# Kernel tuning notes

Hardware: AMD Instinct MI355X
Metric: run time of the kernel (lower is better)

## Reference

```python
import jax, jax.numpy as jnp
import numpy as np

N = 100000
E = 3_200_000
H = 64
R = 2
NEG = 0.01   # leaky_relu default slope
EPS = 1e-5   # BatchNorm eps


def leaky(x):
    return jnp.where(x > 0, x, NEG * x)


def bn(x, g, b, m, v):
    # BatchNorm1d in eval mode (running statistics)
    return (x - m) * jax.lax.rsqrt(v + EPS) * g + b


def setup_inputs() -> dict:
    key = jax.random.key(0)
    ks = jax.random.split(key, 16)
    d = {}
    d["des"] = jax.random.normal(ks[0], (N, 768), jnp.float32)
    d["num"] = jax.random.normal(ks[1], (N, 5), jnp.float32)
    d["cat"] = jax.random.normal(ks[2], (N, 6), jnp.float32)
    d["edge_index"] = jax.random.randint(ks[3], (2, E), 0, N)
    d["edge_type"] = jax.random.randint(ks[4], (E,), 0, R)

    def lin(k, o, i):
        return (jax.random.normal(k, (o, i), jnp.float32) / np.float32(np.sqrt(i)))

    # projection heads: Linear + BatchNorm1d params
    d["des_W"] = lin(ks[5], H, 768); d["des_b"] = jnp.zeros((H,), jnp.float32)
    d["num_W"] = lin(ks[6], H, 5);   d["num_b"] = jnp.zeros((H,), jnp.float32)
    d["cat_W"] = lin(ks[7], H, 6);   d["cat_b"] = jnp.zeros((H,), jnp.float32)
    for name, kk in (("des", ks[8]), ("num", ks[9]), ("cat", ks[10])):
        d[name + "_g"] = jnp.ones((H,), jnp.float32)
        d[name + "_beta"] = jnp.zeros((H,), jnp.float32)
        d[name + "_m"] = 0.1 * jax.random.normal(kk, (H,), jnp.float32)
        d[name + "_v"] = jnp.ones((H,), jnp.float32)
    # RGCN relation weights [R, in, out] (used as F.linear(x, W[r]) -> x @ W[r].T)
    d["rgcn_W"] = jax.random.normal(ks[11], (R, H, H), jnp.float32) / np.float32(np.sqrt(H))
    # classifier
    d["cls_W1"] = lin(ks[12], H // 2, H); d["cls_b1"] = jnp.zeros((H // 2,), jnp.float32)
    d["cls_W2"] = lin(ks[13], 2, H // 2); d["cls_b2"] = jnp.zeros((2,), jnp.float32)
    return d


def reference(des, num, cat, edge_index, edge_type,
              des_W, des_b, des_g, des_beta, des_m, des_v,
              num_W, num_b, num_g, num_beta, num_m, num_v,
              cat_W, cat_b, cat_g, cat_beta, cat_m, cat_v,
              rgcn_W, cls_W1, cls_b1, cls_W2, cls_b2):
    # feature fusion: three Linear+BN+LeakyReLU branches summed
    x = leaky(bn(des @ des_W.T + des_b, des_g, des_beta, des_m, des_v))
    x = x + leaky(bn(num @ num_W.T + num_b, num_g, num_beta, num_m, num_v))
    x = x + leaky(bn(cat @ cat_W.T + cat_b, cat_g, cat_beta, cat_m, cat_v))

    # SimpleRGCNConv: per-relation linear transform + masked scatter-mean over edges
    src, dst = edge_index[0], edge_index[1]  # PyG: row=source, col=target
    n = x.shape[0]
    acc = jnp.zeros((n, H), x.dtype)
    for r in range(R):
        x_r = x @ rgcn_W[r].T                       # F.linear(x, weight[r])
        mask = (edge_type == r).astype(x.dtype)     # [E]
        msg = x_r[src] * mask[:, None]              # gather + mask
        s = jax.ops.segment_sum(msg, dst, num_segments=n)
        cnt = jax.ops.segment_sum(mask, dst, num_segments=n)
        acc = acc + s / jnp.maximum(cnt, 1.0)[:, None]  # mean; 0 for isolated nodes
    x = leaky(acc / R)  # mean over relations

    # dropout in eval mode is identity; classifier
    h = leaky(x @ cls_W1.T + cls_b1)
    return h @ cls_W2.T + cls_b2
```

## Files before the change

### kernel.cpp

```cpp
#include <hip/hip_runtime.h>

typedef unsigned int u32;
typedef unsigned short u16;

#define NEG 0.01f
#define BN_EPS 1e-5f

typedef __attribute__((ext_vector_type(8))) short bf16x8;
typedef __attribute__((ext_vector_type(4))) float f32x4;

__device__ __forceinline__ float bl(u32 u){ union { u32 i; float f; } c; c.i = u << 16; return c.f; }
__device__ __forceinline__ float bh(u32 u){ union { u32 i; float f; } c; c.i = u & 0xFFFF0000u; return c.f; }
__device__ __forceinline__ u16 f2b(float f){
  union { float f; u32 i; } c; c.f = f;
  u32 t = c.i + 0x7FFFu + ((c.i >> 16) & 1u);
  return (u16)(t >> 16);
}
__device__ __forceinline__ float leaky(float v){ return v > 0.f ? v : NEG * v; }

__global__ __launch_bounds__(256) void k_hist_prep(
    const int* __restrict__ ei, const int* __restrict__ et, int E, int HB,
    int* __restrict__ deg2,
    const float* __restrict__ desWf, const float* __restrict__ rgcnW,
    const float* __restrict__ W1, u16* __restrict__ tab)
{
  int bid = blockIdx.x;
  if (bid < HB) {
    int e = bid * 256 + threadIdx.x;
    if (e < E) atomicAdd(&deg2[ei[E + e] * 2 + et[e]], 1);
  } else {
    int i = (bid - HB) * 256 + threadIdx.x;
    if (i < 49152) {
      int j = i & 7, lane = (i >> 3) & 63, t = (i >> 9) & 3, k = i >> 11;
      int row = 16 * t + (lane & 15);
      int col = 32 * k + 8 * (lane >> 4) + j;
      tab[i] = f2b(desWf[row * 768 + col]);
    } else if (i < 57344) {
      int j = i - 49152;
      int h = j >> 7, k = j & 127;
      tab[i] = f2b(rgcnW[(k >= 64 ? 4096 : 0) + h * 64 + (k & 63)]);
    } else if (i < 59392) {
      tab[i] = f2b(W1[i - 57344]);
    }
  }
}

__global__ __launch_bounds__(256) void k_scanA(
    const int* __restrict__ deg2, int* __restrict__ psum, int M)
{
  __shared__ int ws4[4];
  const int tid = threadIdx.x, lane = tid & 63, w = tid >> 6;
  int idx = blockIdx.x * 1024 + tid * 4;
  int4 v = {0, 0, 0, 0};
  if (idx < M) v = *(const int4*)(deg2 + idx);
  int s = v.x + v.y + v.z + v.w;
  #pragma unroll
  for (int o = 1; o < 64; o <<= 1) s += __shfl_xor(s, o);
  if (lane == 0) ws4[w] = s;
  __syncthreads();
  if (tid == 0) psum[blockIdx.x] = ws4[0] + ws4[1] + ws4[2] + ws4[3];
}

__global__ __launch_bounds__(256) void k_scanB(
    const int* __restrict__ psum, int* __restrict__ poff, int NCH)
{
  __shared__ int wsum[4];
  const int tid = threadIdx.x, lane = tid & 63, w = tid >> 6;
  int v = (tid < NCH) ? psum[tid] : 0;
  int s = v;
  #pragma unroll
  for (int o = 1; o < 64; o <<= 1) { int t = __shfl_up(s, o); if (lane >= o) s += t; }
  if (lane == 63) wsum[w] = s;
  __syncthreads();
  if (tid == 0) {
    int a = wsum[0];
    a += wsum[1]; wsum[1] = a;
    a += wsum[2]; wsum[2] = a;
    a += wsum[3]; wsum[3] = a;
  }
  __syncthreads();
  int wbase = (w == 0) ? 0 : wsum[w - 1];
  if (tid < NCH) poff[tid] = wbase + (s - v);
}

__global__ __launch_bounds__(256) void k_scanC(
    const int* __restrict__ deg2, const int* __restrict__ poff,
    int* __restrict__ offs2, int M, int E)
{
  __shared__ int wsum[4];
  const int tid = threadIdx.x, lane = tid & 63, w = tid >> 6;
  int idx = blockIdx.x * 1024 + tid * 4;
  int4 v = {0, 0, 0, 0};
  if (idx < M) v = *(const int4*)(deg2 + idx);
  int s4 = v.x + v.y + v.z + v.w;
  int s = s4;
  #pragma unroll
  for (int o = 1; o < 64; o <<= 1) { int t = __shfl_up(s, o); if (lane >= o) s += t; }
  if (lane == 63) wsum[w] = s;
  __syncthreads();
  if (tid == 0) {
    int a = wsum[0];
    a += wsum[1]; wsum[1] = a;
    a += wsum[2]; wsum[2] = a;
    a += wsum[3]; wsum[3] = a;
  }
  __syncthreads();
  int wbase = (w == 0) ? 0 : wsum[w - 1];
  int ebase = poff[blockIdx.x] + wbase + (s - s4);
  if (idx < M) {
    int4 o4;
    o4.x = ebase;
    o4.y = ebase + v.x;
    o4.z = ebase + v.x + v.y;
    o4.w = ebase + v.x + v.y + v.z;
    *(int4*)(offs2 + idx) = o4;
  }
  if (blockIdx.x == 0 && tid == 0) offs2[M] = E;
}

__global__ __launch_bounds__(256) void k_fuse(
    const float* __restrict__ des, const float* __restrict__ nump, const float* __restrict__ catp,
    const u16* __restrict__ Wpk, const float* __restrict__ desB,
    const float* __restrict__ numW, const float* __restrict__ numB,
    const float* __restrict__ catW, const float* __restrict__ catB,
    const float* __restrict__ dg, const float* __restrict__ dbe, const float* __restrict__ dm, const float* __restrict__ dv,
    const float* __restrict__ ng, const float* __restrict__ nbe, const float* __restrict__ nm, const float* __restrict__ nv,
    const float* __restrict__ cg, const float* __restrict__ cbe, const float* __restrict__ cm, const float* __restrict__ cv,
    u16* __restrict__ x16, int n)
{
  const int tid  = threadIdx.x;
  const int lane = tid & 63;
  const int w    = tid >> 6;

  __shared__ float ync[64][66];
  __shared__ __align__(16) u16 atile[64 * 136];

  const int quad = lane >> 4;
  const int l15  = lane & 15;
  const int fb   = blockIdx.x;
  const int rowbase = fb * 64 + 16 * w;

  {
    float nw[5], cw[6];
    #pragma unroll
    for (int j = 0; j < 5; ++j) nw[j] = numW[lane * 5 + j];
    #pragma unroll
    for (int j = 0; j < 6; ++j) cw[j] = catW[lane * 6 + j];
    float An = ng[lane] * rsqrtf(nv[lane] + BN_EPS);
    float Bn = (numB[lane] - nm[lane]) * An + nbe[lane];
    float Ac = cg[lane] * rsqrtf(cv[lane] + BN_EPS);
    float Bc = (catB[lane] - cm[lane]) * Ac + cbe[lane];
    for (int m = 0; m < 16; ++m) {
      int node = rowbase + m; if (node > n - 1) node = n - 1;
      float yn = 0.f, yc = 0.f;
      #pragma unroll
      for (int j = 0; j < 5; ++j) yn = fmaf(nump[node * 5 + j], nw[j], yn);
      #pragma unroll
      for (int j = 0; j < 6; ++j) yc = fmaf(catp[node * 6 + j], cw[j], yc);
      ync[16 * w + m][lane] = leaky(yn * An + Bn) + leaky(yc * Ac + Bc);
    }
  }

  float Ad4[4], Bd4[4];
  #pragma unroll
  for (int t = 0; t < 4; ++t) {
    int nn = 16 * t + l15;
    float A = dg[nn] * rsqrtf(dv[nn] + BN_EPS);
    Ad4[t] = A;
    Bd4[t] = (desB[nn] - dm[nn]) * A + dbe[nn];
  }
  __syncthreads();

  const u16* bP = Wpk + lane * 8;

  f32x4 acc[4];
  #pragma unroll
  for (int t = 0; t < 4; ++t) acc[t] = (f32x4){0.f, 0.f, 0.f, 0.f};

  const int blk64 = fb * 64;
  for (int tile = 0; tile < 6; ++tile) {
    if (tile > 0) __syncthreads();
    #pragma unroll
    for (int it = 0; it < 4; ++it) {
      int j  = it * 256 + tid;
      int r  = j >> 4;
      int sg = j & 15;
      int row = blk64 + r; if (row > n - 1) row = n - 1;
      const float* p = des + (size_t)row * 768 + tile * 128 + sg * 8;
      float4 u = *(const float4*)p;
      float4 v = *(const float4*)(p + 4);
      u32* d = (u32*)(atile + r * 136 + sg * 8);
      d[0] = (u32)f2b(u.x) | ((u32)f2b(u.y) << 16);
      d[1] = (u32)f2b(u.z) | ((u32)f2b(u.w) << 16);
      d[2] = (u32)f2b(v.x) | ((u32)f2b(v.y) << 16);
      d[3] = (u32)f2b(v.z) | ((u32)f2b(v.w) << 16);
    }
    __syncthreads();
    #pragma unroll
    for (int kk = 0; kk < 4; ++kk) {
      bf16x8 a = *(const bf16x8*)(atile + (16 * w + l15) * 136 + kk * 32 + quad * 8);
      int kg = tile * 4 + kk;
      acc[0] = __builtin_amdgcn_mfma_f32_16x16x32_bf16(a, *(const bf16x8*)(bP + kg * 2048       ), acc[0], 0, 0, 0);
      acc[1] = __builtin_amdgcn_mfma_f32_16x16x32_bf16(a, *(const bf16x8*)(bP + kg * 2048 +  512), acc[1], 0, 0, 0);
      acc[2] = __builtin_amdgcn_mfma_f32_16x16x32_bf16(a, *(const bf16x8*)(bP + kg * 2048 + 1024), acc[2], 0, 0, 0);
      acc[3] = __builtin_amdgcn_mfma_f32_16x16x32_bf16(a, *(const bf16x8*)(bP + kg * 2048 + 1536), acc[3], 0, 0, 0);
    }
  }

  #pragma unroll
  for (int t = 0; t < 4; ++t) {
    #pragma unroll
    for (int r = 0; r < 4; ++r) {
      int m = quad * 4 + r;
      int node = rowbase + m;
      if (node < n) {
        int nn = 16 * t + l15;
        float v = leaky(acc[t][r] * Ad4[t] + Bd4[t]) + ync[16 * w + m][nn];
        x16[(size_t)node * 64 + nn] = f2b(v);
      }
    }
  }
}

__global__ void k_place(const int* __restrict__ ei, const int* __restrict__ et, int E,
                        const int* __restrict__ offs2, int* __restrict__ cur2, int* __restrict__ packed)
{
  int e = blockIdx.x * 256 + threadIdx.x;
  if (e < E) {
    int bin = ei[E + e] * 2 + et[e];
    int pos = offs2[bin] + atomicAdd(&cur2[bin], 1);
    packed[pos] = ei[e];
  }
}

__global__ __launch_bounds__(256) void k_agg(
    const u16* __restrict__ x16, const int* __restrict__ offs2, const int* __restrict__ packed,
    u32* __restrict__ agg, int n)
{
  const int tid = threadIdx.x, lane = tid & 63, w = tid >> 6;
  const int c = lane & 31, half = lane >> 5;

  for (int nd = blockIdx.x * 4 + w; nd < n; nd += gridDim.x * 4) {
    int o0 = offs2[nd * 2], o1 = offs2[nd * 2 + 1], o2 = offs2[nd * 2 + 2];
    float aE[2], aO[2];

    #pragma unroll
    for (int rel = 0; rel < 2; ++rel) {
      int beg = rel ? o1 : o0;
      int end = rel ? o2 : o1;
      float accE = 0.f, accO = 0.f;
      for (int j0 = beg; j0 < end; j0 += 64) {
        int idx = j0 + lane;
        int p = (idx < end) ? packed[idx] : 0;
        p = (p < 0) ? 0 : ((p > n - 1) ? (n - 1) : p);
        int cn = end - j0; if (cn > 64) cn = 64;
        int t = 0;
        for (; t + 16 <= cn; t += 16) {
          int s0 = __shfl(p, t      + half);
          int s1 = __shfl(p, t + 2  + half);
          int s2 = __shfl(p, t + 4  + half);
          int s3 = __shfl(p, t + 6  + half);
          int s4 = __shfl(p, t + 8  + half);
          int s5 = __shfl(p, t + 10 + half);
          int s6 = __shfl(p, t + 12 + half);
          int s7 = __shfl(p, t + 14 + half);
          u32 v0 = *(const u32*)(x16 + (size_t)s0 * 64 + 2 * c);
          u32 v1 = *(const u32*)(x16 + (size_t)s1 * 64 + 2 * c);
          u32 v2 = *(const u32*)(x16 + (size_t)s2 * 64 + 2 * c);
          u32 v3 = *(const u32*)(x16 + (size_t)s3 * 64 + 2 * c);
          u32 v4 = *(const u32*)(x16 + (size_t)s4 * 64 + 2 * c);
          u32 v5 = *(const u32*)(x16 + (size_t)s5 * 64 + 2 * c);
          u32 v6 = *(const u32*)(x16 + (size_t)s6 * 64 + 2 * c);
          u32 v7 = *(const u32*)(x16 + (size_t)s7 * 64 + 2 * c);
          accE += ((bl(v0) + bl(v1)) + (bl(v2) + bl(v3))) + ((bl(v4) + bl(v5)) + (bl(v6) + bl(v7)));
          accO += ((bh(v0) + bh(v1)) + (bh(v2) + bh(v3))) + ((bh(v4) + bh(v5)) + (bh(v6) + bh(v7)));
        }
        for (; t + 8 <= cn; t += 8) {
          int s0 = __shfl(p, t     + half);
          int s1 = __shfl(p, t + 2 + half);
          int s2 = __shfl(p, t + 4 + half);
          int s3 = __shfl(p, t + 6 + half);
          u32 v0 = *(const u32*)(x16 + (size_t)s0 * 64 + 2 * c);
          u32 v1 = *(const u32*)(x16 + (size_t)s1 * 64 + 2 * c);
          u32 v2 = *(const u32*)(x16 + (size_t)s2 * 64 + 2 * c);
          u32 v3 = *(const u32*)(x16 + (size_t)s3 * 64 + 2 * c);
          accE += (bl(v0) + bl(v1)) + (bl(v2) + bl(v3));
          accO += (bh(v0) + bh(v1)) + (bh(v2) + bh(v3));
        }
        for (; t + 2 <= cn; t += 2) {
          int s0 = __shfl(p, t + half);
          u32 v0 = *(const u32*)(x16 + (size_t)s0 * 64 + 2 * c);
          accE += bl(v0); accO += bh(v0);
        }
        if (t < cn) {
          int s0 = __shfl(p, t);
          if (half == 0) {
            u32 v0 = *(const u32*)(x16 + (size_t)s0 * 64 + 2 * c);
            accE += bl(v0); accO += bh(v0);
          }
        }
      }
      accE += __shfl_xor(accE, 32);
      accO += __shfl_xor(accO, 32);
      int cnt = end - beg;
      float sc = 1.f / (float)(cnt > 1 ? cnt : 1);
      aE[rel] = accE * sc;
      aO[rel] = accO * sc;
    }

    float sE = half ? aE[1] : aE[0];
    float sO = half ? aO[1] : aO[0];
    agg[(size_t)nd * 64 + lane] = (u32)f2b(sE) | ((u32)f2b(sO) << 16);
  }
}

__global__ __launch_bounds__(256) void k_mlp(
    const u32* __restrict__ agg, const u16* __restrict__ Wmlp, const u16* __restrict__ W1p,
    const float* __restrict__ b1, const float* __restrict__ W2, const float* __restrict__ b2,
    float2* __restrict__ out, int n)
{
  __shared__ __align__(16) u16 h1[4][16][72];
  __shared__ float h2[4][16][34];

  const int tid = threadIdx.x, lane = tid & 63, w = tid >> 6;
  const int quad = lane >> 4, l15 = lane & 15;
  const int rowbase = blockIdx.x * 64 + 16 * w;

  int rowA = rowbase + l15; if (rowA > n - 1) rowA = n - 1;
  const u16* aRow = (const u16*)(agg + (size_t)rowA * 64);

  f32x4 acc[4];
  #pragma unroll
  for (int t = 0; t < 4; ++t) acc[t] = (f32x4){0.f, 0.f, 0.f, 0.f};
  #pragma unroll
  for (int ks = 0; ks < 4; ++ks) {
    bf16x8 a = *(const bf16x8*)(aRow + ks * 32 + quad * 8);
    #pragma unroll
    for (int t = 0; t < 4; ++t) {
      bf16x8 b = *(const bf16x8*)(Wmlp + (size_t)(16 * t + l15) * 128 + ks * 32 + quad * 8);
      acc[t] = __builtin_amdgcn_mfma_f32_16x16x32_bf16(a, b, acc[t], 0, 0, 0);
    }
  }
  #pragma unroll
  for (int t = 0; t < 4; ++t)
    #pragma unroll
    for (int r = 0; r < 4; ++r) {
      int m = quad * 4 + r;
      h1[w][m][16 * t + l15] = f2b(leaky(0.5f * acc[t][r]));
    }
  __syncthreads();

  f32x4 acc2[2];
  acc2[0] = (f32x4){0.f, 0.f, 0.f, 0.f};
  acc2[1] = (f32x4){0.f, 0.f, 0.f, 0.f};
  #pragma unroll
  for (int ks = 0; ks < 2; ++ks) {
    bf16x8 a = *(const bf16x8*)(&h1[w][l15][ks * 32 + quad * 8]);
    #pragma unroll
    for (int t = 0; t < 2; ++t) {
      bf16x8 b = *(const bf16x8*)(W1p + (size_t)(16 * t + l15) * 64 + ks * 32 + quad * 8);
      acc2[t] = __builtin_amdgcn_mfma_f32_16x16x32_bf16(a, b, acc2[t], 0, 0, 0);
    }
  }
  #pragma unroll
  for (int t = 0; t < 2; ++t)
    #pragma unroll
    for (int r = 0; r < 4; ++r) {
      int m = quad * 4 + r;
      int j = 16 * t + l15;
      h2[w][m][j] = leaky(acc2[t][r] + b1[j]);
    }
  __syncthreads();

  float t0 = 0.f, t1 = 0.f;
  #pragma unroll
  for (int jj = 0; jj < 8; ++jj) {
    int j = quad * 8 + jj;
    float hv = h2[w][l15][j];
    t0 = fmaf(hv, W2[j], t0);
    t1 = fmaf(hv, W2[32 + j], t1);
  }
  t0 += __shfl_xor(t0, 16); t0 += __shfl_xor(t0, 32);
  t1 += __shfl_xor(t1, 16); t1 += __shfl_xor(t1, 32);
  int node = rowbase + l15;
  if (quad == 0 && node < n) {
    float2 q; q.x = t0 + b2[0]; q.y = t1 + b2[1];
    out[node] = q;
  }
}

extern "C" void kernel_launch(void* const* d_in, const int* in_sizes, int n_in,
                              void* d_out, int out_size, void* d_ws, size_t ws_size,
                              hipStream_t stream)
{
  const float* des  = (const float*)d_in[0];
  const float* nump = (const float*)d_in[1];
  const float* catp = (const float*)d_in[2];
  const int* ei   = (const int*)d_in[3];
  const int* et   = (const int*)d_in[4];
  const float* desW = (const float*)d_in[5];
  const float* desB = (const float*)d_in[6];
  const float* numW = (const float*)d_in[7];
  const float* numB = (const float*)d_in[8];
  const float* catW = (const float*)d_in[9];
  const float* catB = (const float*)d_in[10];
  const float* dg  = (const float*)d_in[11];
  const float* dbe = (const float*)d_in[12];
  const float* dm  = (const float*)d_in[13];
  const float* dv  = (const float*)d_in[14];
  const float* ng  = (const float*)d_in[15];
  const float* nbe = (const float*)d_in[16];
  const float* nm  = (const float*)d_in[17];
  const float* nv  = (const float*)d_in[18];
  const float* cg  = (const float*)d_in[19];
  const float* cbe = (const float*)d_in[20];
  const float* cm  = (const float*)d_in[21];
  const float* cv  = (const float*)d_in[22];
  const float* rgcnW = (const float*)d_in[23];
  const float* W1 = (const float*)d_in[24];
  const float* b1 = (const float*)d_in[25];
  const float* W2 = (const float*)d_in[26];
  const float* b2 = (const float*)d_in[27];

  const int N = in_sizes[1] / 5;
  const int E = in_sizes[4];
  const int M = 2 * N;
  const int NB = (N + 63) / 64;
  const int NCH = (M + 1023) / 1024;

  char* ws = (char*)d_ws;
  u16* tab    = (u16*)ws;                  size_t off = (size_t)59392 * 2;
  off = (off + 255) & ~(size_t)255;
  u16* x16    = (u16*)(ws + off);          off += (size_t)N * 64 * 2;
  u32* agg    = (u32*)(ws + off);          off += (size_t)N * 64 * 4;
  int* deg2   = (int*)(ws + off);          off += (size_t)M * 4;
  int* cur2   = (int*)(ws + off);          off += (size_t)M * 4;
  int* offs2  = (int*)(ws + off);          off += (size_t)(M + 1) * 4;
  off = (off + 255) & ~(size_t)255;
  int* psum   = (int*)(ws + off);          off += (size_t)NCH * 4;
  int* poff   = (int*)(ws + off);          off += (size_t)NCH * 4;
  off = (off + 255) & ~(size_t)255;
  int* packed = (int*)(ws + off);

  u16* Wpk    = tab;
  u16* Wmlp   = tab + 49152;
  u16* W1p    = tab + 57344;

  hipMemsetAsync(deg2, 0, (size_t)M * 8, stream);

  const int HB = (E + 255) / 256;
  const int PB = (59392 + 255) / 256;
  k_hist_prep<<<HB + PB, 256, 0, stream>>>(ei, et, E, HB, deg2, desW, rgcnW, W1, tab);

  k_fuse<<<NB, 256, 0, stream>>>(des, nump, catp, Wpk, desB, numW, numB, catW, catB,
                                 dg, dbe, dm, dv, ng, nbe, nm, nv, cg, cbe, cm, cv,
                                 x16, N);

  k_scanA<<<NCH, 256, 0, stream>>>(deg2, psum, M);
  k_scanB<<<1, 256, 0, stream>>>(psum, poff, NCH);
  k_scanC<<<NCH, 256, 0, stream>>>(deg2, poff, offs2, M, E);

  k_place<<<(E + 255) / 256, 256, 0, stream>>>(ei, et, E, offs2, cur2, packed);
  k_agg<<<2048, 256, 0, stream>>>(x16, offs2, packed, agg, N);
  k_mlp<<<(N + 63) / 64, 256, 0, stream>>>(agg, Wmlp, W1p, b1, W2, b2, (float2*)d_out, N);
}
```

Measured before the change: 872.4 us.

## Merge histogram and weight prep into fused projection kernel, stage des weights in LDS

Merges the edge-degree histogram and the small weight-conversion blocks into the feature projection kernel as extra blocks, removing one kernel launch and the dependency that made the projection wait for the prep kernel. Each projection block now converts the fp32 des weight slice to bf16 into a shared-memory tile per k-tile instead of reading a pre-packed bf16 table. This adds redundant weight conversion and global reads in every projection block and more LDS use, which may lower occupancy. In exchange the histogram atomics can run concurrently with the GEMM.

```diff
diff --git a/kernel.cpp b/kernel.cpp
--- a/kernel.cpp
+++ b/kernel.cpp
@@ -18,126 +18,49 @@
 }
 __device__ __forceinline__ float leaky(float v){ return v > 0.f ? v : NEG * v; }
 
-__global__ __launch_bounds__(256) void k_hist_prep(
-    const int* __restrict__ ei, const int* __restrict__ et, int E, int HB,
-    int* __restrict__ deg2,
-    const float* __restrict__ desWf, const float* __restrict__ rgcnW,
-    const float* __restrict__ W1, u16* __restrict__ tab)
-{
-  int bid = blockIdx.x;
-  if (bid < HB) {
-    int e = bid * 256 + threadIdx.x;
-    if (e < E) atomicAdd(&deg2[ei[E + e] * 2 + et[e]], 1);
-  } else {
-    int i = (bid - HB) * 256 + threadIdx.x;
-    if (i < 49152) {
-      int j = i & 7, lane = (i >> 3) & 63, t = (i >> 9) & 3, k = i >> 11;
-      int row = 16 * t + (lane & 15);
-      int col = 32 * k + 8 * (lane >> 4) + j;
-      tab[i] = f2b(desWf[row * 768 + col]);
-    } else if (i < 57344) {
-      int j = i - 49152;
-      int h = j >> 7, k = j & 127;
-      tab[i] = f2b(rgcnW[(k >= 64 ? 4096 : 0) + h * 64 + (k & 63)]);
-    } else if (i < 59392) {
-      tab[i] = f2b(W1[i - 57344]);
-    }
-  }
-}
-
-__global__ __launch_bounds__(256) void k_scanA(
-    const int* __restrict__ deg2, int* __restrict__ psum, int M)
-{
-  __shared__ int ws4[4];
-  const int tid = threadIdx.x, lane = tid & 63, w = tid >> 6;
-  int idx = blockIdx.x * 1024 + tid * 4;
-  int4 v = {0, 0, 0, 0};
-  if (idx < M) v = *(const int4*)(deg2 + idx);
-  int s = v.x + v.y + v.z + v.w;
-  #pragma unroll
-  for (int o = 1; o < 64; o <<= 1) s += __shfl_xor(s, o);
-  if (lane == 0) ws4[w] = s;
-  __syncthreads();
-  if (tid == 0) psum[blockIdx.x] = ws4[0] + ws4[1] + ws4[2] + ws4[3];
-}
-
-__global__ __launch_bounds__(256) void k_scanB(
-    const int* __restrict__ psum, int* __restrict__ poff, int NCH)
-{
-  __shared__ int wsum[4];
-  const int tid = threadIdx.x, lane = tid & 63, w = tid >> 6;
-  int v = (tid < NCH) ? psum[tid] : 0;
-  int s = v;
-  #pragma unroll
-  for (int o = 1; o < 64; o <<= 1) { int t = __shfl_up(s, o); if (lane >= o) s += t; }
-  if (lane == 63) wsum[w] = s;
-  __syncthreads();
-  if (tid == 0) {
-    int a = wsum[0];
-    a += wsum[1]; wsum[1] = a;
-    a += wsum[2]; wsum[2] = a;
-    a += wsum[3]; wsum[3] = a;
-  }
-  __syncthreads();
-  int wbase = (w == 0) ? 0 : wsum[w - 1];
-  if (tid < NCH) poff[tid] = wbase + (s - v);
-}
-
-__global__ __launch_bounds__(256) void k_scanC(
-    const int* __restrict__ deg2, const int* __restrict__ poff,
-    int* __restrict__ offs2, int M, int E)
-{
-  __shared__ int wsum[4];
-  const int tid = threadIdx.x, lane = tid & 63, w = tid >> 6;
-  int idx = blockIdx.x * 1024 + tid * 4;
-  int4 v = {0, 0, 0, 0};
-  if (idx < M) v = *(const int4*)(deg2 + idx);
-  int s4 = v.x + v.y + v.z + v.w;
-  int s = s4;
-  #pragma unroll
-  for (int o = 1; o < 64; o <<= 1) { int t = __shfl_up(s, o); if (lane >= o) s += t; }
-  if (lane == 63) wsum[w] = s;
-  __syncthreads();
-  if (tid == 0) {
-    int a = wsum[0];
-    a += wsum[1]; wsum[1] = a;
-    a += wsum[2]; wsum[2] = a;
-    a += wsum[3]; wsum[3] = a;
-  }
-  __syncthreads();
-  int wbase = (w == 0) ? 0 : wsum[w - 1];
-  int ebase = poff[blockIdx.x] + wbase + (s - s4);
-  if (idx < M) {
-    int4 o4;
-    o4.x = ebase;
-    o4.y = ebase + v.x;
-    o4.z = ebase + v.x + v.y;
-    o4.w = ebase + v.x + v.y + v.z;
-    *(int4*)(offs2 + idx) = o4;
-  }
-  if (blockIdx.x == 0 && tid == 0) offs2[M] = E;
-}
-
-__global__ __launch_bounds__(256) void k_fuse(
+__global__ __launch_bounds__(256) void k_fuse_hist_prep(
     const float* __restrict__ des, const float* __restrict__ nump, const float* __restrict__ catp,
-    const u16* __restrict__ Wpk, const float* __restrict__ desB,
+    const float* __restrict__ desWf, const float* __restrict__ desB,
     const float* __restrict__ numW, const float* __restrict__ numB,
     const float* __restrict__ catW, const float* __restrict__ catB,
     const float* __restrict__ dg, const float* __restrict__ dbe, const float* __restrict__ dm, const float* __restrict__ dv,
     const float* __restrict__ ng, const float* __restrict__ nbe, const float* __restrict__ nm, const float* __restrict__ nv,
     const float* __restrict__ cg, const float* __restrict__ cbe, const float* __restrict__ cm, const float* __restrict__ cv,
-    u16* __restrict__ x16, int n)
+    u16* __restrict__ x16, int n, int FB,
+    const int* __restrict__ ei, const int* __restrict__ et, int E, int HB,
+    int* __restrict__ deg2,
+    const float* __restrict__ rgcnW, const float* __restrict__ W1, u16* __restrict__ tab)
 {
   const int tid  = threadIdx.x;
+  const int bid  = blockIdx.x;
+
+  if (bid >= FB) {
+    int rb = bid - FB;
+    if (rb < HB) {
+      int e = rb * 256 + tid;
+      if (e < E) atomicAdd(&deg2[ei[E + e] * 2 + et[e]], 1);
+    } else {
+      int i = 49152 + (rb - HB) * 256 + tid;
+      if (i < 57344) {
+        int j = i - 49152;
+        int h = j >> 7, k = j & 127;
+        tab[i] = f2b(rgcnW[(k >= 64 ? 4096 : 0) + h * 64 + (k & 63)]);
+      } else if (i < 59392) {
+        tab[i] = f2b(W1[i - 57344]);
+      }
+    }
+    return;
+  }
+
   const int lane = tid & 63;
   const int w    = tid >> 6;
-
   __shared__ float ync[64][66];
   __shared__ __align__(16) u16 atile[64 * 136];
+  __shared__ __align__(16) u16 btile[64 * 136];
 
   const int quad = lane >> 4;
   const int l15  = lane & 15;
-  const int fb   = blockIdx.x;
+  const int fb   = bid;
   const int rowbase = fb * 64 + 16 * w;
 
   {
@@ -171,8 +94,6 @@
   }
   __syncthreads();
 
-  const u16* bP = Wpk + lane * 8;
-
   f32x4 acc[4];
   #pragma unroll
   for (int t = 0; t < 4; ++t) acc[t] = (f32x4){0.f, 0.f, 0.f, 0.f};
@@ -195,15 +116,28 @@
       d[2] = (u32)f2b(v.x) | ((u32)f2b(v.y) << 16);
       d[3] = (u32)f2b(v.z) | ((u32)f2b(v.w) << 16);
     }
+    #pragma unroll
+    for (int it = 0; it < 4; ++it) {
+      int j  = it * 256 + tid;
+      int r  = j >> 4;
+      int sg = j & 15;
+      const float* p = desWf + (size_t)r * 768 + tile * 128 + sg * 8;
+      float4 u = *(const float4*)p;
+      float4 v = *(const float4*)(p + 4);
+      u32* d = (u32*)(btile + r * 136 + sg * 8);
+      d[0] = (u32)f2b(u.x) | ((u32)f2b(u.y) << 16);
+      d[1] = (u32)f2b(u.z) | ((u32)f2b(u.w) << 16);
+      d[2] = (u32)f2b(v.x) | ((u32)f2b(v.y) << 16);
+      d[3] = (u32)f2b(v.z) | ((u32)f2b(v.w) << 16);
+    }
     __syncthreads();
     #pragma unroll
     for (int kk = 0; kk < 4; ++kk) {
       bf16x8 a = *(const bf16x8*)(atile + (16 * w + l15) * 136 + kk * 32 + quad * 8);
-      int kg = tile * 4 + kk;
-      acc[0] = __builtin_amdgcn_mfma_f32_16x16x32_bf16(a, *(const bf16x8*)(bP + kg * 2048       ), acc[0], 0, 0, 0);
-      acc[1] = __builtin_amdgcn_mfma_f32_16x16x32_bf16(a, *(const bf16x8*)(bP + kg * 2048 +  512), acc[1], 0, 0, 0);
-      acc[2] = __builtin_amdgcn_mfma_f32_16x16x32_bf16(a, *(const bf16x8*)(bP + kg * 2048 + 1024), acc[2], 0, 0, 0);
-      acc[3] = __builtin_amdgcn_mfma_f32_16x16x32_bf16(a, *(const bf16x8*)(bP + kg * 2048 + 1536), acc[3], 0, 0, 0);
+      acc[0] = __builtin_amdgcn_mfma_f32_16x16x32_bf16(a, *(const bf16x8*)(btile + (     l15) * 136 + kk * 32 + quad * 8), acc[0], 0, 0, 0);
+      acc[1] = __builtin_amdgcn_mfma_f32_16x16x32_bf16(a, *(const bf16x8*)(btile + (16 + l15) * 136 + kk * 32 + quad * 8), acc[1], 0, 0, 0);
+      acc[2] = __builtin_amdgcn_mfma_f32_16x16x32_bf16(a, *(const bf16x8*)(btile + (32 + l15) * 136 + kk * 32 + quad * 8), acc[2], 0, 0, 0);
+      acc[3] = __builtin_amdgcn_mfma_f32_16x16x32_bf16(a, *(const bf16x8*)(btile + (48 + l15) * 136 + kk * 32 + quad * 8), acc[3], 0, 0, 0);
     }
   }
 
@@ -220,6 +154,79 @@
       }
     }
   }
+}
+
+__global__ __launch_bounds__(256) void k_scanA(
+    const int* __restrict__ deg2, int* __restrict__ psum, int M)
+{
+  __shared__ int ws4[4];
+  const int tid = threadIdx.x, lane = tid & 63, w = tid >> 6;
+  int idx = blockIdx.x * 1024 + tid * 4;
+  int4 v = {0, 0, 0, 0};
+  if (idx < M) v = *(const int4*)(deg2 + idx);
+  int s = v.x + v.y + v.z + v.w;
+  #pragma unroll
+  for (int o = 1; o < 64; o <<= 1) s += __shfl_xor(s, o);
+  if (lane == 0) ws4[w] = s;
+  __syncthreads();
+  if (tid == 0) psum[blockIdx.x] = ws4[0] + ws4[1] + ws4[2] + ws4[3];
+}
+
+__global__ __launch_bounds__(256) void k_scanB(
+    const int* __restrict__ psum, int* __restrict__ poff, int NCH)
+{
+  __shared__ int wsum[4];
+  const int tid = threadIdx.x, lane = tid & 63, w = tid >> 6;
+  int v = (tid < NCH) ? psum[tid] : 0;
+  int s = v;
+  #pragma unroll
+  for (int o = 1; o < 64; o <<= 1) { int t = __shfl_up(s, o); if (lane >= o) s += t; }
+  if (lane == 63) wsum[w] = s;
+  __syncthreads();
+  if (tid == 0) {
+    int a = wsum[0];
+    a += wsum[1]; wsum[1] = a;
+    a += wsum[2]; wsum[2] = a;
+    a += wsum[3]; wsum[3] = a;
+  }
+  __syncthreads();
+  int wbase = (w == 0) ? 0 : wsum[w - 1];
+  if (tid < NCH) poff[tid] = wbase + (s - v);
+}
+
+__global__ __launch_bounds__(256) void k_scanC(
+    const int* __restrict__ deg2, const int* __restrict__ poff,
+    int* __restrict__ offs2, int M, int E)
+{
+  __shared__ int wsum[4];
+  const int tid = threadIdx.x, lane = tid & 63, w = tid >> 6;
+  int idx = blockIdx.x * 1024 + tid * 4;
+  int4 v = {0, 0, 0, 0};
+  if (idx < M) v = *(const int4*)(deg2 + idx);
+  int s4 = v.x + v.y + v.z + v.w;
+  int s = s4;
+  #pragma unroll
+  for (int o = 1; o < 64; o <<= 1) { int t = __shfl_up(s, o); if (lane >= o) s += t; }
+  if (lane == 63) wsum[w] = s;
+  __syncthreads();
+  if (tid == 0) {
+    int a = wsum[0];
+    a += wsum[1]; wsum[1] = a;
+    a += wsum[2]; wsum[2] = a;
+    a += wsum[3]; wsum[3] = a;
+  }
+  __syncthreads();
+  int wbase = (w == 0) ? 0 : wsum[w - 1];
+  int ebase = poff[blockIdx.x] + wbase + (s - s4);
+  if (idx < M) {
+    int4 o4;
+    o4.x = ebase;
+    o4.y = ebase + v.x;
+    o4.z = ebase + v.x + v.y;
+    o4.w = ebase + v.x + v.y + v.z;
+    *(int4*)(offs2 + idx) = o4;
+  }
+  if (blockIdx.x == 0 && tid == 0) offs2[M] = E;
 }
 
 __global__ void k_place(const int* __restrict__ ei, const int* __restrict__ et, int E,
@@ -442,19 +449,17 @@
   off = (off + 255) & ~(size_t)255;
   int* packed = (int*)(ws + off);
 
-  u16* Wpk    = tab;
   u16* Wmlp   = tab + 49152;
   u16* W1p    = tab + 57344;
 
   hipMemsetAsync(deg2, 0, (size_t)M * 8, stream);
 
   const int HB = (E + 255) / 256;
-  const int PB = (59392 + 255) / 256;
-  k_hist_prep<<<HB + PB, 256, 0, stream>>>(ei, et, E, HB, deg2, desW, rgcnW, W1, tab);
-
-  k_fuse<<<NB, 256, 0, stream>>>(des, nump, catp, Wpk, desB, numW, numB, catW, catB,
-                                 dg, dbe, dm, dv, ng, nbe, nm, nv, cg, cbe, cm, cv,
-                                 x16, N);
+  const int PB2 = 40;
+  k_fuse_hist_prep<<<NB + HB + PB2, 256, 0, stream>>>(
+      des, nump, catp, desW, desB, numW, numB, catW, catB,
+      dg, dbe, dm, dv, ng, nbe, nm, nv, cg, cbe, cm, cv,
+      x16, N, NB, ei, et, E, HB, deg2, rgcnW, W1, tab);
 
   k_scanA<<<NCH, 256, 0, stream>>>(deg2, psum, M);
   k_scanB<<<1, 256, 0, stream>>>(psum, poff, NCH);
```

New measurement: 852.6 us. 2.3% less time.
